# Kernel optimization log

Measured on AMD Instinct MI355X. Metric: run time of the kernel, lower is better.

## Reference

```python
import jax, jax.numpy as jnp
import numpy as np

N = 100_000      # nodes
E = 1_600_000    # edges (avg degree 16)
EMB = 32         # embedding_n
VOCAB = 100_000  # nodes_feats_size


def setup_inputs() -> dict:
    key = jax.random.key(0)
    ks = jax.random.split(key, 12)
    s = 1.0 / np.sqrt(EMB)
    return dict(
        features=jax.random.randint(ks[0], (N,), 0, VOCAB),
        cars=jax.random.uniform(ks[1], (N, 1), dtype=jnp.float32),
        entered=jax.random.uniform(ks[2], (N, 1), dtype=jnp.float32),
        free=jax.random.randint(ks[3], (N, 1), 0, 2).astype(jnp.float32),
        src=jax.random.randint(ks[4], (E,), 0, N),
        dst=jax.random.randint(ks[5], (E,), 0, N),
        embed_table=jax.random.normal(ks[6], (VOCAB, EMB), jnp.float32),
        W2n=jax.random.normal(ks[7], (EMB + 1, 1), jnp.float32) * s,
        b2n=jnp.zeros((1,), jnp.float32),
        W2e=jax.random.normal(ks[8], (2 * EMB, EMB), jnp.float32) * s,
        b2e=jnp.zeros((EMB,), jnp.float32),
        W3=jax.random.normal(ks[9], (EMB + 3, 8), jnp.float32) * s,
        b3=jnp.zeros((8,), jnp.float32),
        W4=jax.random.normal(ks[10], (8, 1), jnp.float32) * s,
        b4=jnp.zeros((1,), jnp.float32),
    )


def reference(features, cars, entered, free, src, dst,
              embed_table, W2n, b2n, W2e, b2e, W3, b3, W4, b4):
    relu = jax.nn.relu
    # --- apply_nodes: PredictParkingModule ---
    emb = embed_table[features]                                   # [N, EMB]
    parked = jnp.concatenate([emb, cars], axis=1) @ W2n + b2n     # [N, 1]
    cars1 = relu(relu(parked) + cars)                             # updated 'cars'
    # --- apply_edges: PredictEdgeProbModule ---
    he = jnp.concatenate([emb[src], emb[dst]], axis=1) @ W2e + b2e          # [E, EMB]
    h = relu(jnp.concatenate([he, cars1[src], cars1[dst], entered[src]], axis=1) @ W3 + b3)
    h = h @ W4 + b4                                                          # [E, 1]
    selfloop = (features[src] == features[dst]).astype(jnp.float32)[:, None]  # [E, 1]
    enabled = (selfloop != free[src]).astype(jnp.float32)                     # [E, 1]
    logit = relu(h) * enabled                                                 # [E, 1]
    # --- group_apply_edges(group_by='src'): per-source softmax over edges ---
    l = logit[:, 0]
    m = jax.lax.stop_gradient(jax.ops.segment_max(l, src, num_segments=N))
    ex = jnp.exp(l - m[src])
    ssum = jax.ops.segment_sum(ex, src, num_segments=N)
    prob = (ex / ssum[src])[:, None]                              # [E, 1]
    # --- pull: flow_message_func + flow_reduce_func (sum over dst) ---
    c = cars1[src] * prob                                         # all moving
    o = c * (1.0 - selfloop)                                      # outer
    cars_out = jax.ops.segment_sum(c, dst, num_segments=N)        # [N, 1]
    entered_out = jax.ops.segment_sum(o, dst, num_segments=N)     # [N, 1]
    return cars_out, emb, entered_out
```

## Files before the change

kernel.cpp:

```cpp
#include <hip/hip_runtime.h>
#include <stdint.h>

typedef _Float16 f16x8 __attribute__((ext_vector_type(8)));

#define RBITS 9
#define RSZ   512
#define G     1024
#define MAXB  256
#define CHMAX 1568
#define RMAX  7

__device__ __forceinline__ uint32_t scanExcl256(uint32_t v, uint32_t* wtot, int t)
{
    uint32_t x = v;
    #pragma unroll
    for (int d = 1; d < 64; d <<= 1) {
        uint32_t y = __shfl_up(x, d, 64);
        if ((t & 63) >= d) x += y;
    }
    int w = t >> 6;
    if ((t & 63) == 63) wtot[w] = x;
    __syncthreads();
    uint32_t pre = 0;
    #pragma unroll
    for (int k = 0; k < 4; ++k) pre += (k < w) ? wtot[k] : 0;
    return pre + x - v;
}

__global__ __launch_bounds__(256) void nodecount_kernel(
    const int*   __restrict__ features,
    const float* __restrict__ cars,
    const float* __restrict__ entered,
    const float* __restrict__ free_,
    const float* __restrict__ embed_table,
    const float* __restrict__ W2n,
    const float* __restrict__ b2n,
    const float* __restrict__ W2e,
    const float* __restrict__ W3,
    const int* __restrict__ src, const int* __restrict__ dst,
    float* __restrict__ emb_out,
    float* __restrict__ cars1,
    f16x8* __restrict__ Ah,
    f16x8* __restrict__ Bh,
    float* __restrict__ sfree,
    uint32_t* __restrict__ cntS, uint32_t* __restrict__ cntD,
    int N, int E, int B)
{
    __shared__ uint32_t cS[MAXB], cD[MAXB];
    int t = threadIdx.x, g = blockIdx.x;
    for (int i = t; i < MAXB; i += 256) { cS[i] = 0; cD[i] = 0; }
    __syncthreads();
    int per = (E + G - 1) / G;
    int lo = g * per, hi = min(E, lo + per);
    for (int i = lo + t; i < hi; i += 256) {
        atomicAdd(&cS[src[i] >> RBITS], 1u);
        atomicAdd(&cD[dst[i] >> RBITS], 1u);
    }
    __syncthreads();
    for (int i = t; i < B; i += 256) {
        cntS[(size_t)i * G + g] = cS[i];
        cntD[(size_t)i * G + g] = cD[i];
    }

    if (g * 256 >= N) return;
    __shared__ float Wa[256], Wb[256];
    {
        int k = t >> 3, j = t & 7;
        float a = 0.f, b = 0.f;
        #pragma unroll
        for (int m = 0; m < 32; ++m) {
            float w3 = W3[m * 8 + j];
            a += W2e[k * 32 + m]        * w3;
            b += W2e[(32 + k) * 32 + m] * w3;
        }
        Wa[t] = a;
        Wb[t] = b;
    }
    __syncthreads();

    int i = g * 256 + t;
    if (i >= N) return;
    int f = features[i];
    const float4* erow = (const float4*)(embed_table + (size_t)f * 32);
    float4* orow = (float4*)(emb_out + (size_t)i * 32);
    float e[32];
    #pragma unroll
    for (int q = 0; q < 8; ++q) {
        float4 v = erow[q];
        orow[q] = v;
        e[4*q+0] = v.x; e[4*q+1] = v.y; e[4*q+2] = v.z; e[4*q+3] = v.w;
    }
    float parked = b2n[0];
    #pragma unroll
    for (int k = 0; k < 32; ++k) parked += e[k] * W2n[k];
    float c = cars[i];
    parked += c * W2n[32];
    float c1 = fmaxf(fmaxf(parked, 0.f) + c, 0.f);
    cars1[i] = c1;
    float fm = (float)f + 1.f;
    sfree[i] = (free_[i] > 0.5f) ? -fm : fm;

    float ent = entered[i];
    float a8[8], b8[8];
    #pragma unroll
    for (int j = 0; j < 8; ++j) {
        a8[j] = c1 * W3[32*8 + j] + ent * W3[34*8 + j];
        b8[j] = c1 * W3[33*8 + j];
    }
    #pragma unroll
    for (int k = 0; k < 32; ++k) {
        float x = e[k];
        #pragma unroll
        for (int j = 0; j < 8; ++j) {
            a8[j] += x * Wa[k*8 + j];
            b8[j] += x * Wb[k*8 + j];
        }
    }
    f16x8 av, bv;
    #pragma unroll
    for (int j = 0; j < 8; ++j) { av[j] = (_Float16)a8[j]; bv[j] = (_Float16)b8[j]; }
    Ah[i] = av;
    Bh[i] = bv;
}

__global__ __launch_bounds__(512) void scanA_kernel(
    uint32_t* __restrict__ cntS, uint32_t* __restrict__ cntD,
    uint32_t* __restrict__ totS, uint32_t* __restrict__ totD, int B)
{
    __shared__ uint32_t sh[512];
    int arr = (int)(blockIdx.x >= (unsigned)B);
    int b = blockIdx.x - (arr ? B : 0);
    uint32_t* a   = arr ? cntD : cntS;
    uint32_t* tot = arr ? totD : totS;
    int t = threadIdx.x;
    size_t base = (size_t)b * G + (size_t)t * 2;
    uint32_t v0 = a[base], v1 = a[base + 1];
    uint32_t p = v0 + v1;
    sh[t] = p;
    __syncthreads();
    for (int d = 1; d < 512; d <<= 1) {
        uint32_t u = (t >= d) ? sh[t - d] : 0;
        __syncthreads();
        sh[t] += u;
        __syncthreads();
    }
    uint32_t exc = sh[t] - p;
    a[base] = exc;
    a[base + 1] = exc + v0;
    if (t == 511) tot[b] = sh[t];
}

__global__ __launch_bounds__(256) void scatter_kernel(
    const int* __restrict__ src, const int* __restrict__ dst,
    const float* __restrict__ sfree,
    const f16x8* __restrict__ Ah, const f16x8* __restrict__ Bh,
    const float* __restrict__ b2e, const float* __restrict__ W3,
    const float* __restrict__ b3,  const float* __restrict__ W4,
    const float* __restrict__ b4,
    const uint32_t* __restrict__ cntS, const uint32_t* __restrict__ cntD,
    const uint32_t* __restrict__ totS, const uint32_t* __restrict__ totD,
    uint32_t* __restrict__ payloadS,
    uint32_t* __restrict__ DLa,
    uint16_t* __restrict__ DHa,
    int E, int B)
{
    __shared__ float b3p[8];
    __shared__ uint32_t curS[MAXB], curD[MAXB];
    __shared__ uint32_t tblS[MAXB], tblD[MAXB];
    __shared__ uint32_t wtot[4];
    __shared__ uint32_t buf[CHMAX];
    __shared__ uint16_t bid[CHMAX];

    int t = threadIdx.x, g = blockIdx.x;
    uint32_t vS = (t < B) ? totS[t] : 0;
    uint32_t eS = scanExcl256(vS, wtot, t);
    __syncthreads();
    uint32_t vD = (t < B) ? totD[t] : 0;
    uint32_t eD = scanExcl256(vD, wtot, t);
    if (t < B) {
        curS[t] = eS + cntS[(size_t)t * G + g];
        curD[t] = eD + cntD[(size_t)t * G + g];
    }
    tblS[t] = 0; tblD[t] = 0;
    if (t < 8) {
        float s = b3[t];
        #pragma unroll
        for (int m = 0; m < 32; ++m) s += b2e[m] * W3[m * 8 + t];
        b3p[t] = s;
    }
    __syncthreads();
    float w4[8]; float bias4 = b4[0];
    #pragma unroll
    for (int j = 0; j < 8; ++j) w4[j] = W4[j];

    int per = (E + G - 1) / G;
    int lo = g * per, hi = min(E, lo + per), n = hi - lo;

    uint32_t regA[RMAX], regB[RMAX], regC[RMAX];
    #pragma unroll
    for (int r = 0; r < RMAX; ++r) {
        int idx = r * 256 + t;
        if (idx < n) {
            int i = lo + idx;
            int s = src[i], d = dst[i];
            f16x8 av = Ah[s], bv = Bh[d];
            float fsv = sfree[s];
            float fdv = sfree[d];
            float out = bias4;
            #pragma unroll
            for (int j = 0; j < 8; ++j)
                out += fmaxf((float)av[j] + (float)bv[j] + b3p[j], 0.f) * w4[j];
            bool self  = (fabsf(fsv) == fabsf(fdv));
            bool freeS = (fsv < 0.f);
            float l = (self != freeS) ? fmaxf(out, 0.f) : 0.f;
            float ex = __expf(l);
            uint32_t exb = (uint32_t)__builtin_bit_cast(unsigned short, (_Float16)ex);
            uint32_t keyS = (uint32_t)s >> RBITS;
            uint32_t keyD = (uint32_t)d >> RBITS;
            uint32_t rankS = atomicAdd(&tblS[keyS], 1u);
            uint32_t rankD = atomicAdd(&tblD[keyD], 1u);
            regA[r] = keyS | (rankS << 8) | (self ? 0x80000000u : 0u);
            regB[r] = keyD | (rankD << 8) | ((uint32_t)(d & (RSZ - 1)) << 21);
            regC[r] = (uint32_t)(s & (RSZ - 1)) | (exb << 16);
        }
    }
    __syncthreads();
    uint32_t hS = tblS[t], hD = tblD[t];
    __syncthreads();
    uint32_t bS = scanExcl256(hS, wtot, t);
    __syncthreads();
    uint32_t bD = scanExcl256(hD, wtot, t);
    tblS[t] = bS;
    tblD[t] = bD;
    __syncthreads();

    #pragma unroll
    for (int r = 0; r < RMAX; ++r) {
        int idx = r * 256 + t;
        if (idx < n) {
            uint32_t key = regA[r] & 255u;
            uint32_t slot = tblS[key] + ((regA[r] >> 8) & 0x7FFu);
            buf[slot] = regC[r];
            bid[slot] = (uint16_t)key;
        }
    }
    __syncthreads();
    for (int j = t; j < n; j += 256) {
        uint32_t b = bid[j];
        payloadS[curS[b] + (j - tblS[b])] = buf[j];
    }
    __syncthreads();

    #pragma unroll
    for (int r = 0; r < RMAX; ++r) {
        int idx = r * 256 + t;
        if (idx < n) {
            uint32_t key = regB[r] & 255u;
            uint32_t slot = tblD[key] + ((regB[r] >> 8) & 0x7FFu);
            uint32_t s = ((regA[r] & 255u) << RBITS) | (regC[r] & (RSZ - 1));
            buf[slot] = s | (((regB[r] >> 21) & 0x1FFu) << 17)
                      | (regA[r] & 0x80000000u);
            bid[slot] = (uint16_t)key;
        }
    }
    __syncthreads();
    for (int j = t; j < n; j += 256) {
        uint32_t b = bid[j];
        DLa[curD[b] + (j - tblD[b])] = buf[j];
    }
    __syncthreads();

    #pragma unroll
    for (int r = 0; r < RMAX; ++r) {
        int idx = r * 256 + t;
        if (idx < n) {
            uint32_t key = regB[r] & 255u;
            uint32_t slot = tblD[key] + ((regB[r] >> 8) & 0x7FFu);
            buf[slot] = regC[r] >> 16;
        }
    }
    __syncthreads();
    for (int j = t; j < n; j += 256) {
        uint32_t b = bid[j];
        DHa[curD[b] + (j - tblD[b])] = (uint16_t)buf[j];
    }
}

__global__ __launch_bounds__(256) void bucketS_kernel(
    const uint32_t* __restrict__ totS, const uint32_t* __restrict__ payloadS,
    const float* __restrict__ cars1, float* __restrict__ ratio,
    int N, int B)
{
    __shared__ float acc[RSZ];
    __shared__ uint32_t wtot[4];
    __shared__ uint32_t be[2];
    int b = blockIdx.x, t = threadIdx.x;
    uint32_t v = (t < B) ? totS[t] : 0;
    uint32_t e = scanExcl256(v, wtot, t);
    if (t == b) { be[0] = e; be[1] = e + v; }
    for (int i = t; i < RSZ; i += 256) acc[i] = 0.f;
    __syncthreads();
    uint32_t beg = be[0], end = be[1];
    for (uint32_t i = beg + t; i < end; i += 256) {
        uint32_t p = payloadS[i];
        float val = (float)__builtin_bit_cast(_Float16, (unsigned short)(p >> 16));
        atomicAdd(&acc[p & (RSZ - 1)], val);
    }
    __syncthreads();
    int nb = b << RBITS;
    for (int i = t; i < RSZ; i += 256) {
        int node = nb + i;
        if (node < N) {
            float s = acc[i];
            ratio[node] = cars1[node] / (s > 0.f ? s : 1.f);
        }
    }
}

__global__ __launch_bounds__(256) void bucketD_kernel(
    const uint32_t* __restrict__ totD,
    const uint32_t* __restrict__ DLa, const uint16_t* __restrict__ DHa,
    const float* __restrict__ ratio,
    float* __restrict__ cars_out, float* __restrict__ entered_out,
    int N, int B)
{
    __shared__ float accC[RSZ], accX[RSZ];
    __shared__ uint32_t wtot[4];
    __shared__ uint32_t be[2];
    int b = blockIdx.x, t = threadIdx.x;
    uint32_t v = (t < B) ? totD[t] : 0;
    uint32_t e = scanExcl256(v, wtot, t);
    if (t == b) { be[0] = e; be[1] = e + v; }
    for (int i = t; i < RSZ; i += 256) { accC[i] = 0.f; accX[i] = 0.f; }
    __syncthreads();
    uint32_t beg = be[0], end = be[1];
    for (uint32_t i = beg + t; i < end; i += 256) {
        uint32_t m = DLa[i];
        float ex = (float)__builtin_bit_cast(_Float16, (unsigned short)DHa[i]);
        int s  = m & 0x1FFFF;
        int ld = (m >> 17) & (RSZ - 1);
        float c = ratio[s] * ex;
        atomicAdd(&accC[ld], c);
        if (m & 0x80000000u) atomicAdd(&accX[ld], c);
    }
    __syncthreads();
    int nb = b << RBITS;
    for (int i = t; i < RSZ; i += 256) {
        int node = nb + i;
        if (node < N) {
            float cs = accC[i];
            cars_out[node]    = cs;
            entered_out[node] = cs - accX[i];
        }
    }
}

extern "C" void kernel_launch(void* const* d_in, const int* in_sizes, int n_in,
                              void* d_out, int out_size, void* d_ws, size_t ws_size,
                              hipStream_t stream)
{
    const int N = in_sizes[0];
    const int E = in_sizes[4];
    const int B = (N + RSZ - 1) / RSZ;
    const int L = B * G;

    const int*   features    = (const int*)  d_in[0];
    const float* cars        = (const float*)d_in[1];
    const float* entered     = (const float*)d_in[2];
    const float* free_       = (const float*)d_in[3];
    const int*   src         = (const int*)  d_in[4];
    const int*   dst         = (const int*)  d_in[5];
    const float* embed_table = (const float*)d_in[6];
    const float* W2n         = (const float*)d_in[7];
    const float* b2n         = (const float*)d_in[8];
    const float* W2e         = (const float*)d_in[9];
    const float* b2e         = (const float*)d_in[10];
    const float* W3          = (const float*)d_in[11];
    const float* b3          = (const float*)d_in[12];
    const float* W4          = (const float*)d_in[13];
    const float* b4          = (const float*)d_in[14];

    float* out         = (float*)d_out;
    float* cars_out    = out;
    float* emb_out     = out + N;
    float* entered_out = out + (size_t)N * 33;

    float*    ws       = (float*)d_ws;
    float*    cars1    = ws;
    float*    ratio    = ws + N;
    float*    sfree    = ws + (size_t)2 * N;
    f16x8*    Ah       = (f16x8*)(ws + (size_t)4 * N);
    f16x8*    Bh       = (f16x8*)(ws + (size_t)8 * N);
    uint32_t* cntS     = (uint32_t*)(ws + (size_t)12 * N);
    uint32_t* cntD     = cntS + L;
    uint32_t* totS     = cntD + L;
    uint32_t* totD     = totS + MAXB;
    uint32_t* payloadS = totD + MAXB;
    uint32_t* DLa      = payloadS + E;
    uint16_t* DHa      = (uint16_t*)(DLa + E);

    nodecount_kernel<<<G, 256, 0, stream>>>(
        features, cars, entered, free_, embed_table, W2n, b2n, W2e, W3,
        src, dst, emb_out, cars1, Ah, Bh, sfree, cntS, cntD, N, E, B);
    scanA_kernel<<<2 * B, 512, 0, stream>>>(cntS, cntD, totS, totD, B);
    scatter_kernel<<<G, 256, 0, stream>>>(
        src, dst, sfree, Ah, Bh, b2e, W3, b3, W4, b4,
        cntS, cntD, totS, totD, payloadS, DLa, DHa, E, B);
    bucketS_kernel<<<B, 256, 0, stream>>>(totS, payloadS, cars1, ratio, N, B);
    bucketD_kernel<<<B, 256, 0, stream>>>(
        totD, DLa, DHa, ratio, cars_out, entered_out, N, B);
}
```

Measured before the change: 100.2 us.

## Merge dst metadata and exponent into 64-bit records, halve scatter grid

The dst-side index word and the fp16 exponent are now packed into one 64-bit record. This replaces two separate arrays and drops one LDS staging pass, with its barriers, in the scatter kernel. The grid for counting and scatter shrinks from 1024 to 512 blocks, so each block handles bigger chunks (CHMAX/RMAX raised), and the per-block bucket counts are stored as uint16, which shrinks the count matrix and makes the scan one element per thread. The trade-offs are fewer blocks for latency hiding, more registers per thread for the larger unrolled chunk, and counts that only fit because per-bucket totals stay below 65536.

```diff
diff --git a/kernel.cpp b/kernel.cpp
--- a/kernel.cpp
+++ b/kernel.cpp
@@ -5,10 +5,10 @@
 
 #define RBITS 9
 #define RSZ   512
-#define G     1024
+#define G     512
 #define MAXB  256
-#define CHMAX 1568
-#define RMAX  7
+#define CHMAX 3200
+#define RMAX  13
 
 __device__ __forceinline__ uint32_t scanExcl256(uint32_t v, uint32_t* wtot, int t)
 {
@@ -43,7 +43,7 @@
     f16x8* __restrict__ Ah,
     f16x8* __restrict__ Bh,
     float* __restrict__ sfree,
-    uint32_t* __restrict__ cntS, uint32_t* __restrict__ cntD,
+    uint16_t* __restrict__ cntS, uint16_t* __restrict__ cntD,
     int N, int E, int B)
 {
     __shared__ uint32_t cS[MAXB], cD[MAXB];
@@ -58,8 +58,8 @@
     }
     __syncthreads();
     for (int i = t; i < B; i += 256) {
-        cntS[(size_t)i * G + g] = cS[i];
-        cntD[(size_t)i * G + g] = cD[i];
+        cntS[(size_t)i * G + g] = (uint16_t)cS[i];
+        cntD[(size_t)i * G + g] = (uint16_t)cD[i];
     }
 
     if (g * 256 >= N) return;
@@ -124,30 +124,26 @@
 }
 
 __global__ __launch_bounds__(512) void scanA_kernel(
-    uint32_t* __restrict__ cntS, uint32_t* __restrict__ cntD,
+    uint16_t* __restrict__ cntS, uint16_t* __restrict__ cntD,
     uint32_t* __restrict__ totS, uint32_t* __restrict__ totD, int B)
 {
-    __shared__ uint32_t sh[512];
+    __shared__ uint32_t sh[G];
     int arr = (int)(blockIdx.x >= (unsigned)B);
     int b = blockIdx.x - (arr ? B : 0);
-    uint32_t* a   = arr ? cntD : cntS;
+    uint16_t* a   = arr ? cntD : cntS;
     uint32_t* tot = arr ? totD : totS;
     int t = threadIdx.x;
-    size_t base = (size_t)b * G + (size_t)t * 2;
-    uint32_t v0 = a[base], v1 = a[base + 1];
-    uint32_t p = v0 + v1;
-    sh[t] = p;
-    __syncthreads();
-    for (int d = 1; d < 512; d <<= 1) {
+    uint32_t v = a[(size_t)b * G + t];
+    sh[t] = v;
+    __syncthreads();
+    for (int d = 1; d < G; d <<= 1) {
         uint32_t u = (t >= d) ? sh[t - d] : 0;
         __syncthreads();
         sh[t] += u;
         __syncthreads();
     }
-    uint32_t exc = sh[t] - p;
-    a[base] = exc;
-    a[base + 1] = exc + v0;
-    if (t == 511) tot[b] = sh[t];
+    a[(size_t)b * G + t] = (uint16_t)(sh[t] - v);
+    if (t == G - 1) tot[b] = sh[t];
 }
 
 __global__ __launch_bounds__(256) void scatter_kernel(
@@ -157,18 +153,17 @@
     const float* __restrict__ b2e, const float* __restrict__ W3,
     const float* __restrict__ b3,  const float* __restrict__ W4,
     const float* __restrict__ b4,
-    const uint32_t* __restrict__ cntS, const uint32_t* __restrict__ cntD,
+    const uint16_t* __restrict__ cntS, const uint16_t* __restrict__ cntD,
     const uint32_t* __restrict__ totS, const uint32_t* __restrict__ totD,
     uint32_t* __restrict__ payloadS,
-    uint32_t* __restrict__ DLa,
-    uint16_t* __restrict__ DHa,
+    uint64_t* __restrict__ metaEx,
     int E, int B)
 {
     __shared__ float b3p[8];
     __shared__ uint32_t curS[MAXB], curD[MAXB];
     __shared__ uint32_t tblS[MAXB], tblD[MAXB];
     __shared__ uint32_t wtot[4];
-    __shared__ uint32_t buf[CHMAX];
+    __shared__ union { uint32_t b32[CHMAX]; uint64_t b64[CHMAX]; } stg;
     __shared__ uint16_t bid[CHMAX];
 
     int t = threadIdx.x, g = blockIdx.x;
@@ -239,15 +234,15 @@
         int idx = r * 256 + t;
         if (idx < n) {
             uint32_t key = regA[r] & 255u;
-            uint32_t slot = tblS[key] + ((regA[r] >> 8) & 0x7FFu);
-            buf[slot] = regC[r];
+            uint32_t slot = tblS[key] + ((regA[r] >> 8) & 0xFFFu);
+            stg.b32[slot] = regC[r];
             bid[slot] = (uint16_t)key;
         }
     }
     __syncthreads();
     for (int j = t; j < n; j += 256) {
         uint32_t b = bid[j];
-        payloadS[curS[b] + (j - tblS[b])] = buf[j];
+        payloadS[curS[b] + (j - tblS[b])] = stg.b32[j];
     }
     __syncthreads();
 
@@ -256,33 +251,18 @@
         int idx = r * 256 + t;
         if (idx < n) {
             uint32_t key = regB[r] & 255u;
-            uint32_t slot = tblD[key] + ((regB[r] >> 8) & 0x7FFu);
+            uint32_t slot = tblD[key] + ((regB[r] >> 8) & 0xFFFu);
             uint32_t s = ((regA[r] & 255u) << RBITS) | (regC[r] & (RSZ - 1));
-            buf[slot] = s | (((regB[r] >> 21) & 0x1FFu) << 17)
-                      | (regA[r] & 0x80000000u);
+            uint32_t mlo = s | (((regB[r] >> 21) & 0x1FFu) << 17)
+                         | (regA[r] & 0x80000000u);
+            stg.b64[slot] = (uint64_t)mlo | ((uint64_t)(regC[r] >> 16) << 32);
             bid[slot] = (uint16_t)key;
         }
     }
     __syncthreads();
     for (int j = t; j < n; j += 256) {
         uint32_t b = bid[j];
-        DLa[curD[b] + (j - tblD[b])] = buf[j];
-    }
-    __syncthreads();
-
-    #pragma unroll
-    for (int r = 0; r < RMAX; ++r) {
-        int idx = r * 256 + t;
-        if (idx < n) {
-            uint32_t key = regB[r] & 255u;
-            uint32_t slot = tblD[key] + ((regB[r] >> 8) & 0x7FFu);
-            buf[slot] = regC[r] >> 16;
-        }
-    }
-    __syncthreads();
-    for (int j = t; j < n; j += 256) {
-        uint32_t b = bid[j];
-        DHa[curD[b] + (j - tblD[b])] = (uint16_t)buf[j];
+        metaEx[curD[b] + (j - tblD[b])] = stg.b64[j];
     }
 }
 
@@ -319,7 +299,7 @@
 
 __global__ __launch_bounds__(256) void bucketD_kernel(
     const uint32_t* __restrict__ totD,
-    const uint32_t* __restrict__ DLa, const uint16_t* __restrict__ DHa,
+    const uint64_t* __restrict__ metaEx,
     const float* __restrict__ ratio,
     float* __restrict__ cars_out, float* __restrict__ entered_out,
     int N, int B)
@@ -335,8 +315,9 @@
     __syncthreads();
     uint32_t beg = be[0], end = be[1];
     for (uint32_t i = beg + t; i < end; i += 256) {
-        uint32_t m = DLa[i];
-        float ex = (float)__builtin_bit_cast(_Float16, (unsigned short)DHa[i]);
+        uint64_t me = metaEx[i];
+        uint32_t m = (uint32_t)me;
+        float ex = (float)__builtin_bit_cast(_Float16, (unsigned short)(me >> 32));
         int s  = m & 0x1FFFF;
         int ld = (m >> 17) & (RSZ - 1);
         float c = ratio[s] * ex;
@@ -391,22 +372,21 @@
     float*    sfree    = ws + (size_t)2 * N;
     f16x8*    Ah       = (f16x8*)(ws + (size_t)4 * N);
     f16x8*    Bh       = (f16x8*)(ws + (size_t)8 * N);
-    uint32_t* cntS     = (uint32_t*)(ws + (size_t)12 * N);
-    uint32_t* cntD     = cntS + L;
-    uint32_t* totS     = cntD + L;
+    uint32_t* totS     = (uint32_t*)(ws + (size_t)12 * N);
     uint32_t* totD     = totS + MAXB;
-    uint32_t* payloadS = totD + MAXB;
-    uint32_t* DLa      = payloadS + E;
-    uint16_t* DHa      = (uint16_t*)(DLa + E);
+    uint64_t* metaEx   = (uint64_t*)(totD + MAXB);
+    uint32_t* payloadS = (uint32_t*)(metaEx + E);
+    uint16_t* cntS     = (uint16_t*)(payloadS + E);
+    uint16_t* cntD     = cntS + L;
 
     nodecount_kernel<<<G, 256, 0, stream>>>(
         features, cars, entered, free_, embed_table, W2n, b2n, W2e, W3,
         src, dst, emb_out, cars1, Ah, Bh, sfree, cntS, cntD, N, E, B);
-    scanA_kernel<<<2 * B, 512, 0, stream>>>(cntS, cntD, totS, totD, B);
+    scanA_kernel<<<2 * B, G, 0, stream>>>(cntS, cntD, totS, totD, B);
     scatter_kernel<<<G, 256, 0, stream>>>(
         src, dst, sfree, Ah, Bh, b2e, W3, b3, W4, b4,
-        cntS, cntD, totS, totD, payloadS, DLa, DHa, E, B);
+        cntS, cntD, totS, totD, payloadS, metaEx, E, B);
     bucketS_kernel<<<B, 256, 0, stream>>>(totS, payloadS, cars1, ratio, N, B);
     bucketD_kernel<<<B, 256, 0, stream>>>(
-        totD, DLa, DHa, ratio, cars_out, entered_out, N, B);
-}
+        totD, metaEx, ratio, cars_out, entered_out, N, B);
+}
```

Result: faster. 98.20 us (-2.0%).
